# Kernel optimization log

Hardware: AMD Instinct MI355X
Metric: run time of the kernel (lower is better)

Reference implementation:

```python
import jax, jax.numpy as jnp
import numpy as np

NUM_HEAD = 8   # in_channels // 64 for in_channels=512
DIM = 8        # per-head dim (== num_head in this module)
H_CH = NUM_HEAD * DIM  # 64
SCALE = DIM ** (-0.5)


def _conv(x, w, b, padding):
    # x: [N,C,H,W], w: [O,I,kh,kw]
    out = jax.lax.conv_general_dilated(
        x, w, window_strides=(1, 1), padding=padding,
        dimension_numbers=("NCHW", "OIHW", "NCHW"))
    return out + b[None, :, None, None]


def setup_inputs() -> dict:
    key = jax.random.key(0)
    ks = jax.random.split(key, 4)
    N, C, H, W = 4, 512, 48, 48
    x = jax.random.normal(ks[0], (N, C, H, W), dtype=jnp.float32)
    qkv_w = jax.random.normal(ks[1], (3 * H_CH, C, 1, 1), dtype=jnp.float32) * 0.05
    qkv_b = jnp.zeros((3 * H_CH,), dtype=jnp.float32)
    pos_w = jax.random.normal(ks[2], (H_CH, H_CH, 3, 3), dtype=jnp.float32) * 0.05
    pos_b = jnp.zeros((H_CH,), dtype=jnp.float32)
    res_w = jax.random.normal(ks[3], (C, H_CH, 1, 1), dtype=jnp.float32) * 0.05
    res_b = jnp.zeros((C,), dtype=jnp.float32)
    return {"x": x, "qkv_w": qkv_w, "qkv_b": qkv_b,
            "pos_w": pos_w, "pos_b": pos_b,
            "res_w": res_w, "res_b": res_b}


def reference(x, qkv_w, qkv_b, pos_w, pos_b, res_w, res_b):
    N, C, H, W = x.shape
    L = H * W
    # 1x1 conv QKV projection -> [N, 3h, H, W]
    qkv = _conv(x, qkv_w, qkv_b, "VALID")
    # [N, num_head, 3*dim, L]
    qkv = qkv.reshape(N, NUM_HEAD, 3 * DIM, L)
    q, k, v = qkv[:, :, :DIM], qkv[:, :, DIM:2 * DIM], qkv[:, :, 2 * DIM:]
    # attn = q^T @ k * scale : [N, nh, L, L], softmax over keys (last dim)
    attn = jnp.einsum("nhdq,nhdk->nhqk", q, k) * SCALE
    attn = jax.nn.softmax(attn, axis=-1)
    # out = v @ attn^T : [N, nh, dim, L]
    out = jnp.einsum("nhdk,nhqk->nhdq", v, attn)
    out = out.reshape(N, H_CH, H, W)
    # positional branch: 3x3 conv on v
    pos = _conv(v.reshape(N, H_CH, H, W), pos_w, pos_b, "SAME")
    out = out + pos
    # resume 1x1 conv -> [N, out_channels, H, W]
    return _conv(out, res_w, res_b, "VALID")
```

## Files before the change

### kernel.cpp

```cpp
#include <hip/hip_runtime.h>

#define L_ATT 2304
#define QSCALE_LOG2E 0.5100695712f

using bh8 = __attribute__((ext_vector_type(8))) short;
using f4  = __attribute__((ext_vector_type(4))) float;

#if __has_builtin(__builtin_amdgcn_exp2f)
#define EXP2(x) __builtin_amdgcn_exp2f(x)
#else
#define EXP2(x) exp2f(x)
#endif

__device__ inline short f2b(float f) {
    union { float f; unsigned u; } c; c.f = f;
    unsigned r = (c.u + 0x7FFFu + ((c.u >> 16) & 1u)) >> 16;
    return (short)r;
}
__device__ inline float b2f(short s) {
    union { unsigned u; float f; } c;
    c.u = ((unsigned)(unsigned short)s) << 16;
    return c.f;
}
__device__ inline int packhi(float lo, float hi) {
    return (int)__builtin_amdgcn_perm(__float_as_uint(hi), __float_as_uint(lo), 0x07060302u);
}

__global__ __launch_bounds__(256) void prep_kernel(
    const float* __restrict__ x, const float* __restrict__ qkv_w,
    const float* __restrict__ res_w, const float* __restrict__ pos_w,
    short* __restrict__ xt, short* __restrict__ wqb,
    short* __restrict__ reswb, short* __restrict__ wqp)
{
    __shared__ float s[64][68];
    const int g = blockIdx.x;
    if (g < 272) {
        int j = g * 256 + threadIdx.x;
        if (j < 24576) {
            float4 v = ((const float4*)qkv_w)[j];
            short4 o = { f2b(v.x), f2b(v.y), f2b(v.z), f2b(v.w) };
            *(short4*)(wqb + (size_t)j * 4) = o;
        } else if (j < 32768) {
            int idx = j - 24576;
            float4 v = ((const float4*)res_w)[idx];
            short4 o = { f2b(v.x), f2b(v.y), f2b(v.z), f2b(v.w) };
            *(short4*)(reswb + (size_t)idx * 4) = o;
        } else {
            int e = j - 32768;
            wqp[e] = f2b(pos_w[(size_t)(e & 4095) * 9 + (e >> 12)]);
        }
        return;
    }
    const int gg = g - 272;
    const int l0 = (gg % 36) * 64, k0 = ((gg / 36) & 7) * 64, n = gg / 288;
    const int tr = threadIdx.x >> 4, tc4 = (threadIdx.x & 15) * 4;
    const float* xp = x + ((size_t)n * 512 + k0) * L_ATT + l0;
#pragma unroll
    for (int r = 0; r < 4; ++r)
        *(float4*)&s[tr + r * 16][tc4] =
            *(const float4*)(xp + (size_t)(tr + r * 16) * L_ATT + tc4);
    __syncthreads();
    short* op = xt + ((size_t)n * L_ATT + l0) * 512 + k0;
#pragma unroll
    for (int r = 0; r < 4; ++r) {
        int l = tr + r * 16;
        short4 o = { f2b(s[tc4 + 0][l]), f2b(s[tc4 + 1][l]),
                     f2b(s[tc4 + 2][l]), f2b(s[tc4 + 3][l]) };
        *(short4*)(op + (size_t)l * 512 + tc4) = o;
    }
}

__global__ __launch_bounds__(256) void qkv_kernel(
    const short* __restrict__ xt, const short* __restrict__ wqb,
    const float* __restrict__ qkv_b, short* __restrict__ qt8,
    short* __restrict__ kt8, short* __restrict__ vt, short* __restrict__ vle)
{
    const int g = blockIdx.x;
    const int xcd = g & 7, rr = g >> 3;
    const int y = rr % 3, grp = rr / 3;
    const int code = grp * 8 + xcd;
    const int l0 = (code % 36) * 64, oc0 = y * 64, n = code / 36;

    const int lane = threadIdx.x & 63, wave = threadIdx.x >> 6;
    const int col = lane & 15, quad = lane >> 4;
    const int ocb = oc0 + wave * 16;

    f4 acc[4];
#pragma unroll
    for (int nt = 0; nt < 4; ++nt) acc[nt] = (f4){0.f, 0.f, 0.f, 0.f};

    const short* arow = wqb + (size_t)(ocb + col) * 512 + quad * 8;
    const short* brow = xt + ((size_t)n * L_ATT + l0 + col) * 512 + quad * 8;

#pragma unroll 4
    for (int k0 = 0; k0 < 512; k0 += 32) {
        bh8 af = *(const bh8*)(arow + k0);
        bh8 b0 = *(const bh8*)(brow + k0);
        bh8 b1 = *(const bh8*)(brow + (size_t)16 * 512 + k0);
        bh8 b2 = *(const bh8*)(brow + (size_t)32 * 512 + k0);
        bh8 b3 = *(const bh8*)(brow + (size_t)48 * 512 + k0);
        acc[0] = __builtin_amdgcn_mfma_f32_16x16x32_bf16(af, b0, acc[0], 0, 0, 0);
        acc[1] = __builtin_amdgcn_mfma_f32_16x16x32_bf16(af, b1, acc[1], 0, 0, 0);
        acc[2] = __builtin_amdgcn_mfma_f32_16x16x32_bf16(af, b2, acc[2], 0, 0, 0);
        acc[3] = __builtin_amdgcn_mfma_f32_16x16x32_bf16(af, b3, acc[3], 0, 0, 0);
    }

    const int obase = ocb + quad * 4;
    const int h = obase / 24;
    const int r0 = obase - h * 24;
    const int slice = n * 8 + h;

#pragma unroll
    for (int nt = 0; nt < 4; ++nt) {
        int l = l0 + nt * 16 + col;
        float v[4];
#pragma unroll
        for (int reg = 0; reg < 4; ++reg) v[reg] = acc[nt][reg] + qkv_b[obase + reg];
        if (r0 < 8) {
            short4 o = { f2b(v[0] * QSCALE_LOG2E), f2b(v[1] * QSCALE_LOG2E),
                         f2b(v[2] * QSCALE_LOG2E), f2b(v[3] * QSCALE_LOG2E) };
            *(short4*)(qt8 + ((size_t)slice * L_ATT + l) * 8 + r0) = o;
        } else if (r0 < 16) {
            short4 o = { f2b(v[0]), f2b(v[1]), f2b(v[2]), f2b(v[3]) };
            *(short4*)(kt8 + ((size_t)slice * L_ATT + l) * 8 + (r0 - 8)) = o;
        } else {
            short4 o = { f2b(v[0]), f2b(v[1]), f2b(v[2]), f2b(v[3]) };
            int d0 = r0 - 16;
#pragma unroll
            for (int reg = 0; reg < 4; ++reg)
                vt[((size_t)slice * 8 + d0 + reg) * L_ATT + l] = ((short*)&o)[reg];
            *(short4*)(vle + ((size_t)n * L_ATT + l) * 64 + h * 8 + d0) = o;
        }
    }
}

__global__ __launch_bounds__(256) void attnpos_kernel(
    const short* __restrict__ qt8, const short* __restrict__ kt8,
    const short* __restrict__ vt, const short* __restrict__ vle,
    const short* __restrict__ wqp, const float* __restrict__ pbias,
    float* __restrict__ t32, short* __restrict__ pcv)
{
    __shared__ short smem[2064];
    const int g = blockIdx.x;
    const int tid = threadIdx.x;
    const int lane = tid & 63, wave = tid >> 6;
    const int col = lane & 15, quad = lane >> 4;

    if (g < 576) {
        const int h = g & 7, r = g >> 3;
        const int n = r / 18;
        const int q0 = (r % 18) * 128;
        const int slice = n * 8 + h;

        const short* qs  = qt8 + (size_t)slice * L_ATT * 8;
        const short* ks8 = kt8 + (size_t)slice * L_ATT * 8;
        const short* vb  = vt  + (size_t)slice * 8 * L_ATT;

        if (tid < 16) smem[2048 + tid] = (tid < 8) ? (short)0x3F80 : (short)0;

        bh8 zero8 = {0, 0, 0, 0, 0, 0, 0, 0};
        bh8 qf[2];
#pragma unroll
        for (int f = 0; f < 2; ++f) {
            qf[f] = zero8;
            if (quad == 0)
                qf[f] = *(const bh8*)(qs + (size_t)(q0 + wave * 32 + f * 16 + col) * 8);
        }

        const int kxor = (quad == 0) ? 512 : 0;
        int kidx[4];
#pragma unroll
        for (int nt = 0; nt < 4; ++nt)
            kidx[nt] = (quad == 0) ? (nt * 16 + col) * 8 : 2056;
        const int vxor = (col < 8) ? 512 : 0;
        int vidx[2];
#pragma unroll
        for (int ks = 0; ks < 2; ++ks)
            vidx[ks] = (col < 8)
                     ? 1024 + col * 64 + ((ks * 32 + quad * 8 + col * 8) & 63)
                     : ((col == 8) ? 2048 : 2056);

        const int ksl = ((lane >> 5) & 1) * 32 + ((lane >> 2) & 1) * 16
                      + ((lane >> 3) & 3) * 4 + (lane & 3);
        const int vd = lane >> 3, vkc = (lane & 7) * 8;
        const int vsl = 1024 + vd * 64 + ((vkc + vd * 8) & 63);

        if (wave == 0)
            *(uint4*)&smem[ksl * 8] = *(const uint4*)(ks8 + (size_t)lane * 8);
        else if (wave == 1)
            *(uint4*)&smem[vsl] = *(const uint4*)(vb + (size_t)vd * L_ATT + vkc);
        __syncthreads();

        f4 oacc[2];
        oacc[0] = (f4){0.f, 0.f, 0.f, 0.f};
        oacc[1] = (f4){0.f, 0.f, 0.f, 0.f};

        int sofs = 512;
        for (int t = 0; t < 36; ++t) {
            uint4 dk, dv;
            if (wave == 0)
                dk = *(const uint4*)(ks8 + (size_t)((t + 1) * 64 + lane) * 8);
            else if (wave == 1)
                dv = *(const uint4*)(vb + (size_t)vd * L_ATT + (t + 1) * 64 + vkc);

            bh8 kf[4], vf[2];
#pragma unroll
            for (int nt = 0; nt < 4; ++nt) kf[nt] = *(const bh8*)&smem[kidx[nt]];
#pragma unroll
            for (int ks = 0; ks < 2; ++ks) vf[ks] = *(const bh8*)&smem[vidx[ks]];

#pragma unroll
            for (int f = 0; f < 2; ++f) {
                f4 s[4];
#pragma unroll
                for (int nt = 0; nt < 4; ++nt) {
                    f4 z = (f4){0.f, 0.f, 0.f, 0.f};
                    s[nt] = __builtin_amdgcn_mfma_f32_16x16x32_bf16(kf[nt], qf[f], z, 0, 0, 0);
                }
                float e[4][4];
#pragma unroll
                for (int nt = 0; nt < 4; ++nt)
#pragma unroll
                    for (int reg = 0; reg < 4; ++reg)
                        e[nt][reg] = EXP2(s[nt][reg]);
#pragma unroll
                for (int ks = 0; ks < 2; ++ks) {
                    union { int i[4]; bh8 v; } pu;
                    pu.i[0] = packhi(e[2 * ks][0],     e[2 * ks][1]);
                    pu.i[1] = packhi(e[2 * ks][2],     e[2 * ks][3]);
                    pu.i[2] = packhi(e[2 * ks + 1][0], e[2 * ks + 1][1]);
                    pu.i[3] = packhi(e[2 * ks + 1][2], e[2 * ks + 1][3]);
                    oacc[f] = __builtin_amdgcn_mfma_f32_16x16x32_bf16(vf[ks], pu.v, oacc[f], 0, 0, 0);
                }
            }

            if (wave == 0)      *(uint4*)&smem[sofs + ksl * 8] = dk;
            else if (wave == 1) *(uint4*)&smem[sofs + vsl] = dv;

#pragma unroll
            for (int nt = 0; nt < 4; ++nt) kidx[nt] ^= kxor;
            vidx[0] ^= vxor; vidx[1] ^= vxor;
            sofs ^= 512;
            __syncthreads();
        }

#pragma unroll
        for (int f = 0; f < 2; ++f) {
            float ls = __shfl(oacc[f][0], 32 + col, 64);
            float inv = 1.0f / ls;
            if (quad < 2) {
                int qg = q0 + wave * 32 + f * 16 + col;
                float4 o = { oacc[f][0] * inv, oacc[f][1] * inv,
                             oacc[f][2] * inv, oacc[f][3] * inv };
                *(float4*)(t32 + ((size_t)n * L_ATT + qg) * 64 + h * 8 + quad * 4) = o;
            }
        }
        return;
    }

    const int gf = g - 576;
    const int l0 = (gf % 144) * 16, n = gf / 144;
    const int t = wave;

    const int la = l0 + col;
    const int ya = la / 48, xa = la - ya * 48;

    f4 acc = (f4){0.f, 0.f, 0.f, 0.f};
    const short* vbase = vle + (size_t)n * L_ATT * 64;

#pragma unroll
    for (int q = 0; q < 9; ++q) {
        const int dy = q / 3 - 1, dx = q - (q / 3) * 3 - 1;
        const bool valid = ((unsigned)(ya + dy) < 48u) && ((unsigned)(xa + dx) < 48u);
        const short* ap = vbase + (size_t)(la + dy * 48 + dx) * 64 + quad * 8;
#pragma unroll
        for (int ks = 0; ks < 2; ++ks) {
            bh8 af = {0, 0, 0, 0, 0, 0, 0, 0};
            if (valid) af = *(const bh8*)(ap + ks * 32);
            bh8 bf = *(const bh8*)(wqp + ((size_t)q * 64 + t * 16 + col) * 64
                                   + ks * 32 + quad * 8);
            acc = __builtin_amdgcn_mfma_f32_16x16x32_bf16(af, bf, acc, 0, 0, 0);
        }
    }

    short* op = pcv + (size_t)n * L_ATT * 64;
    const int oc = t * 16 + col;
    const float bb = pbias[oc];
#pragma unroll
    for (int reg = 0; reg < 4; ++reg) {
        int l = l0 + quad * 4 + reg;
        op[(size_t)l * 64 + oc] = f2b(acc[reg] + bb);
    }
}

__global__ __launch_bounds__(256) void res_kernel(
    const float* __restrict__ t32, const short* __restrict__ pcv,
    const short* __restrict__ reswb, const float* __restrict__ res_b,
    float* __restrict__ out)
{
    const int g = blockIdx.x;
    const int xcd = g & 7, rr = g >> 3;
    const int y = rr & 7, grp = rr >> 3;
    const int code = grp * 8 + xcd;
    const int l0 = (code % 36) * 64, oc0 = y * 64, n = code / 36;

    const int lane = threadIdx.x & 63, wave = threadIdx.x >> 6;
    const int col = lane & 15, quad = lane >> 4;
    const int ocb = oc0 + wave * 16;

    f4 acc[4];
#pragma unroll
    for (int nt = 0; nt < 4; ++nt) acc[nt] = (f4){0.f, 0.f, 0.f, 0.f};

#pragma unroll
    for (int ks = 0; ks < 2; ++ks) {
        bh8 af = *(const bh8*)(reswb + (size_t)(ocb + col) * 64 + ks * 32 + quad * 8);
#pragma unroll
        for (int nt = 0; nt < 4; ++nt) {
            const size_t boff = ((size_t)n * L_ATT + l0 + nt * 16 + col) * 64
                              + ks * 32 + quad * 8;
            float4 ta = *(const float4*)(t32 + boff);
            float4 tb = *(const float4*)(t32 + boff + 4);
            bh8 pv = *(const bh8*)(pcv + boff);
            union { int i[4]; bh8 v; } pu;
            pu.i[0] = packhi(ta.x + b2f(pv[0]), ta.y + b2f(pv[1]));
            pu.i[1] = packhi(ta.z + b2f(pv[2]), ta.w + b2f(pv[3]));
            pu.i[2] = packhi(tb.x + b2f(pv[4]), tb.y + b2f(pv[5]));
            pu.i[3] = packhi(tb.z + b2f(pv[6]), tb.w + b2f(pv[7]));
            acc[nt] = __builtin_amdgcn_mfma_f32_16x16x32_bf16(af, pu.v, acc[nt], 0, 0, 0);
        }
    }

#pragma unroll
    for (int nt = 0; nt < 4; ++nt) {
        int l = l0 + nt * 16 + col;
#pragma unroll
        for (int reg = 0; reg < 4; ++reg) {
            int oc = ocb + quad * 4 + reg;
            out[((size_t)n * 512 + oc) * L_ATT + l] = acc[nt][reg] + res_b[oc];
        }
    }
}

extern "C" void kernel_launch(void* const* d_in, const int* in_sizes, int n_in,
                              void* d_out, int out_size, void* d_ws, size_t ws_size,
                              hipStream_t stream)
{
    const float* x      = (const float*)d_in[0];
    const float* qkv_w  = (const float*)d_in[1];
    const float* qkv_b  = (const float*)d_in[2];
    const float* pos_w  = (const float*)d_in[3];
    const float* pos_b  = (const float*)d_in[4];
    const float* res_w  = (const float*)d_in[5];
    const float* res_b  = (const float*)d_in[6];
    float* out = (float*)d_out;

    char* ws = (char*)d_ws;
    short* xt    = (short*)(ws);
    float* t32   = (float*)(ws);
    short* qt8   = (short*)(ws + 9437184);
    short* kt8   = (short*)(ws + 10616832);
    short* vt    = (short*)(ws + 11796480);
    short* pcv   = (short*)(ws + 12976128);
    short* wqb   = (short*)(ws + 14155776);
    short* reswb = (short*)(ws + 14352384);
    short* vle   = (short*)(ws + 14417920);
    short* wqp   = (short*)(ws + 15597568);

    prep_kernel<<<1424, 256, 0, stream>>>(x, qkv_w, res_w, pos_w, xt, wqb, reswb, wqp);
    qkv_kernel<<<432, 256, 0, stream>>>(xt, wqb, qkv_b, qt8, kt8, vt, vle);
    attnpos_kernel<<<1152, 256, 0, stream>>>(qt8, kt8, vt, vle, wqp, pos_b, t32, pcv);
    res_kernel<<<1152, 256, 0, stream>>>(t32, pcv, reswb, res_b, out);
}
```

Before: 158.5 us.

## Split attention over key halves and combine partial softmax in res kernel

Attention blocks now each handle half of the key range, doubling the number of attention workgroups, and write unnormalized numerators and row sums. The final 1x1-conv kernel sums the two partials and normalizes before the projection. The QKV kernel also uses smaller 32-column tiles to launch twice as many blocks. This raises parallelism and occupancy, at the cost of extra partial-buffer traffic and more reads in the res kernel. It relies on the exponentials having no running-max subtraction, so partial sums add directly.

Result: faster. 154.0 us (-2.9%).

```diff
diff --git a/kernel.cpp b/kernel.cpp
--- a/kernel.cpp
+++ b/kernel.cpp
@@ -79,15 +79,15 @@
     const int xcd = g & 7, rr = g >> 3;
     const int y = rr % 3, grp = rr / 3;
     const int code = grp * 8 + xcd;
-    const int l0 = (code % 36) * 64, oc0 = y * 64, n = code / 36;
+    const int l0 = (code % 72) * 32, oc0 = y * 64, n = code / 72;
 
     const int lane = threadIdx.x & 63, wave = threadIdx.x >> 6;
     const int col = lane & 15, quad = lane >> 4;
     const int ocb = oc0 + wave * 16;
 
-    f4 acc[4];
-#pragma unroll
-    for (int nt = 0; nt < 4; ++nt) acc[nt] = (f4){0.f, 0.f, 0.f, 0.f};
+    f4 acc[2];
+    acc[0] = (f4){0.f, 0.f, 0.f, 0.f};
+    acc[1] = (f4){0.f, 0.f, 0.f, 0.f};
 
     const short* arow = wqb + (size_t)(ocb + col) * 512 + quad * 8;
     const short* brow = xt + ((size_t)n * L_ATT + l0 + col) * 512 + quad * 8;
@@ -97,12 +97,8 @@
         bh8 af = *(const bh8*)(arow + k0);
         bh8 b0 = *(const bh8*)(brow + k0);
         bh8 b1 = *(const bh8*)(brow + (size_t)16 * 512 + k0);
-        bh8 b2 = *(const bh8*)(brow + (size_t)32 * 512 + k0);
-        bh8 b3 = *(const bh8*)(brow + (size_t)48 * 512 + k0);
         acc[0] = __builtin_amdgcn_mfma_f32_16x16x32_bf16(af, b0, acc[0], 0, 0, 0);
         acc[1] = __builtin_amdgcn_mfma_f32_16x16x32_bf16(af, b1, acc[1], 0, 0, 0);
-        acc[2] = __builtin_amdgcn_mfma_f32_16x16x32_bf16(af, b2, acc[2], 0, 0, 0);
-        acc[3] = __builtin_amdgcn_mfma_f32_16x16x32_bf16(af, b3, acc[3], 0, 0, 0);
     }
 
     const int obase = ocb + quad * 4;
@@ -111,7 +107,7 @@
     const int slice = n * 8 + h;
 
 #pragma unroll
-    for (int nt = 0; nt < 4; ++nt) {
+    for (int nt = 0; nt < 2; ++nt) {
         int l = l0 + nt * 16 + col;
         float v[4];
 #pragma unroll
@@ -138,7 +134,7 @@
     const short* __restrict__ qt8, const short* __restrict__ kt8,
     const short* __restrict__ vt, const short* __restrict__ vle,
     const short* __restrict__ wqp, const float* __restrict__ pbias,
-    float* __restrict__ t32, short* __restrict__ pcv)
+    float* __restrict__ pnum, float* __restrict__ pls, short* __restrict__ pcv)
 {
     __shared__ short smem[2064];
     const int g = blockIdx.x;
@@ -146,10 +142,13 @@
     const int lane = tid & 63, wave = tid >> 6;
     const int col = lane & 15, quad = lane >> 4;
 
-    if (g < 576) {
+    if (g < 1152) {
         const int h = g & 7, r = g >> 3;
-        const int n = r / 18;
-        const int q0 = (r % 18) * 128;
+        const int n = r / 36;
+        const int rem = r - n * 36;
+        const int qt = rem >> 1, half = rem & 1;
+        const int q0 = qt * 128;
+        const int kbase = half * 1152;
         const int slice = n * 8 + h;
 
         const short* qs  = qt8 + (size_t)slice * L_ATT * 8;
@@ -186,9 +185,9 @@
         const int vsl = 1024 + vd * 64 + ((vkc + vd * 8) & 63);
 
         if (wave == 0)
-            *(uint4*)&smem[ksl * 8] = *(const uint4*)(ks8 + (size_t)lane * 8);
+            *(uint4*)&smem[ksl * 8] = *(const uint4*)(ks8 + (size_t)(kbase + lane) * 8);
         else if (wave == 1)
-            *(uint4*)&smem[vsl] = *(const uint4*)(vb + (size_t)vd * L_ATT + vkc);
+            *(uint4*)&smem[vsl] = *(const uint4*)(vb + (size_t)vd * L_ATT + kbase + vkc);
         __syncthreads();
 
         f4 oacc[2];
@@ -196,12 +195,12 @@
         oacc[1] = (f4){0.f, 0.f, 0.f, 0.f};
 
         int sofs = 512;
-        for (int t = 0; t < 36; ++t) {
+        for (int t = 0; t < 18; ++t) {
             uint4 dk, dv;
             if (wave == 0)
-                dk = *(const uint4*)(ks8 + (size_t)((t + 1) * 64 + lane) * 8);
+                dk = *(const uint4*)(ks8 + (size_t)(kbase + (t + 1) * 64 + lane) * 8);
             else if (wave == 1)
-                dv = *(const uint4*)(vb + (size_t)vd * L_ATT + (t + 1) * 64 + vkc);
+                dv = *(const uint4*)(vb + (size_t)vd * L_ATT + kbase + (t + 1) * 64 + vkc);
 
             bh8 kf[4], vf[2];
 #pragma unroll
@@ -244,21 +243,21 @@
             __syncthreads();
         }
 
+        const size_t prow = (size_t)(slice * 2 + half) * L_ATT;
 #pragma unroll
         for (int f = 0; f < 2; ++f) {
-            float ls = __shfl(oacc[f][0], 32 + col, 64);
-            float inv = 1.0f / ls;
+            int qg = q0 + wave * 32 + f * 16 + col;
             if (quad < 2) {
-                int qg = q0 + wave * 32 + f * 16 + col;
-                float4 o = { oacc[f][0] * inv, oacc[f][1] * inv,
-                             oacc[f][2] * inv, oacc[f][3] * inv };
-                *(float4*)(t32 + ((size_t)n * L_ATT + qg) * 64 + h * 8 + quad * 4) = o;
+                float4 o = { oacc[f][0], oacc[f][1], oacc[f][2], oacc[f][3] };
+                *(float4*)(pnum + (prow + qg) * 8 + quad * 4) = o;
+            } else if (quad == 2) {
+                pls[prow + qg] = oacc[f][0];
             }
         }
         return;
     }
 
-    const int gf = g - 576;
+    const int gf = g - 1152;
     const int l0 = (gf % 144) * 16, n = gf / 144;
     const int t = wave;
 
@@ -294,9 +293,9 @@
 }
 
 __global__ __launch_bounds__(256) void res_kernel(
-    const float* __restrict__ t32, const short* __restrict__ pcv,
-    const short* __restrict__ reswb, const float* __restrict__ res_b,
-    float* __restrict__ out)
+    const float* __restrict__ pnum, const float* __restrict__ pls,
+    const short* __restrict__ pcv, const short* __restrict__ reswb,
+    const float* __restrict__ res_b, float* __restrict__ out)
 {
     const int g = blockIdx.x;
     const int xcd = g & 7, rr = g >> 3;
@@ -315,18 +314,28 @@
 #pragma unroll
     for (int ks = 0; ks < 2; ++ks) {
         bh8 af = *(const bh8*)(reswb + (size_t)(ocb + col) * 64 + ks * 32 + quad * 8);
+        const int h = ks * 4 + quad;
+        const size_t p0 = (size_t)((n * 8 + h) * 2) * L_ATT;
+        const size_t p1 = p0 + L_ATT;
 #pragma unroll
         for (int nt = 0; nt < 4; ++nt) {
-            const size_t boff = ((size_t)n * L_ATT + l0 + nt * 16 + col) * 64
-                              + ks * 32 + quad * 8;
-            float4 ta = *(const float4*)(t32 + boff);
-            float4 tb = *(const float4*)(t32 + boff + 4);
-            bh8 pv = *(const bh8*)(pcv + boff);
+            const int l = l0 + nt * 16 + col;
+            float4 a0 = *(const float4*)(pnum + (p0 + l) * 8);
+            float4 a1 = *(const float4*)(pnum + (p0 + l) * 8 + 4);
+            float4 b0 = *(const float4*)(pnum + (p1 + l) * 8);
+            float4 b1 = *(const float4*)(pnum + (p1 + l) * 8 + 4);
+            float inv = 1.0f / (pls[p0 + l] + pls[p1 + l]);
+            bh8 pv = *(const bh8*)(pcv + ((size_t)n * L_ATT + l) * 64
+                                   + ks * 32 + quad * 8);
             union { int i[4]; bh8 v; } pu;
-            pu.i[0] = packhi(ta.x + b2f(pv[0]), ta.y + b2f(pv[1]));
-            pu.i[1] = packhi(ta.z + b2f(pv[2]), ta.w + b2f(pv[3]));
-            pu.i[2] = packhi(tb.x + b2f(pv[4]), tb.y + b2f(pv[5]));
-            pu.i[3] = packhi(tb.z + b2f(pv[6]), tb.w + b2f(pv[7]));
+            pu.i[0] = packhi((a0.x + b0.x) * inv + b2f(pv[0]),
+                             (a0.y + b0.y) * inv + b2f(pv[1]));
+            pu.i[1] = packhi((a0.z + b0.z) * inv + b2f(pv[2]),
+                             (a0.w + b0.w) * inv + b2f(pv[3]));
+            pu.i[2] = packhi((a1.x + b1.x) * inv + b2f(pv[4]),
+                             (a1.y + b1.y) * inv + b2f(pv[5]));
+            pu.i[3] = packhi((a1.z + b1.z) * inv + b2f(pv[6]),
+                             (a1.w + b1.w) * inv + b2f(pv[7]));
             acc[nt] = __builtin_amdgcn_mfma_f32_16x16x32_bf16(af, pu.v, acc[nt], 0, 0, 0);
         }
     }
@@ -357,7 +366,8 @@
 
     char* ws = (char*)d_ws;
     short* xt    = (short*)(ws);
-    float* t32   = (float*)(ws);
+    float* pnum  = (float*)(ws);
+    float* pls   = (float*)(ws + 4718592);
     short* qt8   = (short*)(ws + 9437184);
     short* kt8   = (short*)(ws + 10616832);
     short* vt    = (short*)(ws + 11796480);
@@ -368,7 +378,7 @@
     short* wqp   = (short*)(ws + 15597568);
 
     prep_kernel<<<1424, 256, 0, stream>>>(x, qkv_w, res_w, pos_w, xt, wqb, reswb, wqp);
-    qkv_kernel<<<432, 256, 0, stream>>>(xt, wqb, qkv_b, qt8, kt8, vt, vle);
-    attnpos_kernel<<<1152, 256, 0, stream>>>(qt8, kt8, vt, vle, wqp, pos_b, t32, pcv);
-    res_kernel<<<1152, 256, 0, stream>>>(t32, pcv, reswb, res_b, out);
-}
+    qkv_kernel<<<864, 256, 0, stream>>>(xt, wqb, qkv_b, qt8, kt8, vt, vle);
+    attnpos_kernel<<<1728, 256, 0, stream>>>(qt8, kt8, vt, vle, wqp, pos_b, pnum, pls, pcv);
+    res_kernel<<<1152, 256, 0, stream>>>(pnum, pls, pcv, reswb, res_b, out);
+}
```
